# Performance work log

Measured on AMD Instinct MI355X. Metric: run time of the kernel, lower is better.

The kernel has to match this reference:

```python
import math
import jax, jax.numpy as jnp
import numpy as np

B, T, C = 4, 2048, 1024
N_HEAD = 16
HEAD_DIM = C // N_HEAD


def setup_inputs() -> dict:
    key = jax.random.key(0)
    k1, k2, k3 = jax.random.split(key, 3)
    x = jax.random.normal(k1, (B, T, C), dtype=jnp.float32)
    # nn.Linear weights: (out_features, in_features); init scale ~1/sqrt(C)
    w_attn = jax.random.normal(k2, (3 * C, C), dtype=jnp.float32) / math.sqrt(C)
    w_proj = jax.random.normal(k3, (C, C), dtype=jnp.float32) / math.sqrt(C)
    return {"x": x, "w_attn": w_attn, "w_proj": w_proj}


def reference(x, w_attn, w_proj):
    Bx, Tx, Cx = x.shape
    qkv = x @ w_attn.T  # (B,T,3C)
    q, k, v = jnp.split(qkv, 3, axis=2)
    # (B,T,H,D) -> (B,H,T,D)
    q = q.reshape(Bx, Tx, N_HEAD, HEAD_DIM).transpose(0, 2, 1, 3)
    k = k.reshape(Bx, Tx, N_HEAD, HEAD_DIM).transpose(0, 2, 1, 3)
    v = v.reshape(Bx, Tx, N_HEAD, HEAD_DIM).transpose(0, 2, 1, 3)
    scale = 1.0 / math.sqrt(HEAD_DIM)
    att = jnp.einsum("bhqd,bhkd->bhqk", q, k) * scale
    causal = jnp.tril(jnp.ones((Tx, Tx), dtype=bool))
    att = jnp.where(causal[None, None, :, :], att, -jnp.inf)
    att = jax.nn.softmax(att, axis=-1)
    out = jnp.einsum("bhqk,bhkd->bhqd", att, v)
    out = out.transpose(0, 2, 1, 3).reshape(Bx, Tx, Cx)
    return out @ w_proj.T
```

## Files before the change

kernel.cpp:

```cpp
#include <hip/hip_runtime.h>
#include <hip/hip_bf16.h>


typedef __attribute__((ext_vector_type(8))) short bf16x8;
typedef __attribute__((ext_vector_type(4))) float f32x4;
typedef __attribute__((ext_vector_type(16))) float f32x16;
typedef unsigned short ushort_t;

#if __has_builtin(__builtin_amdgcn_exp2f)
#define EXP2(x) __builtin_amdgcn_exp2f(x)
#else
#define EXP2(x) exp2f(x)
#endif

__device__ inline ushort_t f2bf(float f) {
    union { float f; unsigned int u; } x; x.f = f;
    return (ushort_t)((x.u + 0x7fffu + ((x.u >> 16) & 1u)) >> 16);
}

__device__ inline ushort_t f2bf_fast(float f) {
    union { float f; unsigned int u; } x; x.f = f;
    return (ushort_t)((x.u + 0x8000u) >> 16);
}

__device__ inline bf16x8 load8_f32_to_bf16(const float* p) {
    float4 f0 = *(const float4*)p;
    float4 f1 = *(const float4*)(p + 4);
    bf16x8 r;
    r[0] = (short)f2bf(f0.x); r[1] = (short)f2bf(f0.y);
    r[2] = (short)f2bf(f0.z); r[3] = (short)f2bf(f0.w);
    r[4] = (short)f2bf(f1.x); r[5] = (short)f2bf(f1.y);
    r[6] = (short)f2bf(f1.z); r[7] = (short)f2bf(f1.w);
    return r;
}

__device__ inline void gl2lds16(const ushort_t* g, ushort_t* l) {
    __builtin_amdgcn_global_load_lds(
        (const __attribute__((address_space(1))) unsigned int*)g,
        (__attribute__((address_space(3))) unsigned int*)l,
        16, 0, 0);
}

__global__ void cvt3(const float* __restrict__ a, long n8a,
                     const float* __restrict__ b, long n8b,
                     const float* __restrict__ c, long n8c,
                     ushort_t* __restrict__ out) {
    long i = (long)blockIdx.x * 256 + threadIdx.x;
    const float* src; long off;
    if (i < n8a) { src = a; off = i; }
    else if (i < n8a + n8b) { src = b; off = i - n8a; }
    else if (i < n8a + n8b + n8c) { src = c; off = i - n8a - n8b; }
    else return;
    *(bf16x8*)(out + i * 8) = load8_f32_to_bf16(src + off * 8);
}

__global__ void fill_zero_f32(float* out, int n) {
    int i = blockIdx.x * 256 + threadIdx.x;
    if (i < n) out[i] = 0.0f;
}

#define BM 128
#define BN 128
#define BK 64

#define QK_LOG2E_SCALE 0.18033688011112042f

template <int EPI>
__global__ __launch_bounds__(256) void gemm_lds(
        const ushort_t* __restrict__ A, const ushort_t* __restrict__ B,
        void* __restrict__ Cp, void* __restrict__ Cp2,
        int M, int N, int K) {
    __shared__ ushort_t As[BM * BK];
    __shared__ ushort_t Bs[BN * BK];

    const int tid  = threadIdx.x;
    const int lane = tid & 63;
    const int w    = tid >> 6;
    const int l31  = lane & 31;
    const int half = lane >> 5;

    const int bm = blockIdx.y * BM;
    const int bn = blockIdx.x * BN;
    const int wm = (w & 1) * 64;
    const int wn = (w >> 1) * 64;

    const int lr8 = lane >> 3;
    const int cbg = ((lane & 7) ^ lr8) * 8;
    const ushort_t* Aw = A + (size_t)(bm + w * 32 + lr8) * K + cbg;
    const ushort_t* Bw = B + (size_t)(bn + w * 32 + lr8) * K + cbg;
    ushort_t* Asw = &As[(w * 32) * BK];
    ushort_t* Bsw = &Bs[(w * 32) * BK];

    f32x16 acc[2][2] = {};

    for (int k0 = 0; k0 < K; k0 += BK) {
        if (k0) __syncthreads();
#pragma unroll
        for (int j = 0; j < 4; j++) {
            gl2lds16(Aw + (size_t)(j * 8) * K + k0, Asw + j * 8 * BK);
            gl2lds16(Bw + (size_t)(j * 8) * K + k0, Bsw + j * 8 * BK);
        }
        __syncthreads();

#pragma unroll
        for (int s = 0; s < 4; s++) {
            const int cs = (((2 * s + half) ^ (lane & 7)) * 8);
            bf16x8 af[2], bfr[2];
#pragma unroll
            for (int i = 0; i < 2; i++)
                af[i] = *(const bf16x8*)&As[(wm + i * 32 + l31) * BK + cs];
#pragma unroll
            for (int i = 0; i < 2; i++)
                bfr[i] = *(const bf16x8*)&Bs[(wn + i * 32 + l31) * BK + cs];
#pragma unroll
            for (int mi = 0; mi < 2; mi++)
#pragma unroll
                for (int ni = 0; ni < 2; ni++)
                    acc[mi][ni] = __builtin_amdgcn_mfma_f32_32x32x16_bf16(
                        af[mi], bfr[ni], acc[mi][ni], 0, 0, 0);
        }
    }

#pragma unroll
    for (int mi = 0; mi < 2; mi++)
#pragma unroll
        for (int ni = 0; ni < 2; ni++) {
            const int colg = bn + wn + ni * 32 + l31;
            if constexpr (EPI == 1) {
                float* cb = (float*)Cp + colg;
#pragma unroll
                for (int r = 0; r < 16; r++) {
                    const int row = bm + wm + mi * 32 + (r & 3) + 8 * (r >> 2) + 4 * half;
                    cb[(size_t)row * N] = acc[mi][ni][r];
                }
            } else {
                if (colg < 2048) {
                    const float qs = (colg < 1024) ? QK_LOG2E_SCALE : 1.0f;
                    ushort_t* cb = (ushort_t*)Cp + colg;
#pragma unroll
                    for (int r = 0; r < 16; r++) {
                        const int row = bm + wm + mi * 32 + (r & 3) + 8 * (r >> 2) + 4 * half;
                        cb[(size_t)row * 2048] = f2bf(acc[mi][ni][r] * qs);
                    }
                } else {
                    const int vc = colg - 2048;
                    const int hh = vc >> 6, dd = vc & 63;
                    ushort_t* vtp = (ushort_t*)Cp2 + ((size_t)hh * 64 + dd) * 2048;
#pragma unroll
                    for (int r = 0; r < 16; r++) {
                        const int row = bm + wm + mi * 32 + (r & 3) + 8 * (r >> 2) + 4 * half;
                        const int bb = row >> 11, tt = row & 2047;
                        vtp[(size_t)bb * 16 * 64 * 2048 + tt] = f2bf(acc[mi][ni][r]);
                    }
                }
            }
        }
}

#define LDK 72

template <bool A_F32, bool B_F32, int EPI>
__global__ __launch_bounds__(256) void gemm_nt(
        const void* __restrict__ Ap, const void* __restrict__ Bp,
        void* __restrict__ Cp, void* __restrict__ Cp2,
        int M, int N, int K) {
    __shared__ ushort_t As[BM * LDK];
    __shared__ ushort_t Bs[BN * LDK];

    const int tid  = threadIdx.x;
    const int lane = tid & 63;
    const int w    = tid >> 6;
    const int quad = lane >> 4;
    const int l16  = lane & 15;

    const int bm = blockIdx.y * BM;
    const int bn = blockIdx.x * BN;
    const int wm = (w & 1) * 64;
    const int wn = (w >> 1) * 64;

    f32x4 acc[4][4] = {};

    const int lrow = tid >> 3;
    const int lcol = (tid & 7) * 8;

    bf16x8 pa[4], pb[4];
#pragma unroll
    for (int i = 0; i < 4; i++) {
        const int ra = lrow + i * 32;
        if constexpr (A_F32)
            pa[i] = load8_f32_to_bf16((const float*)Ap + (size_t)(bm + ra) * K + lcol);
        else
            pa[i] = *(const bf16x8*)((const ushort_t*)Ap + (size_t)(bm + ra) * K + lcol);
        if constexpr (B_F32)
            pb[i] = load8_f32_to_bf16((const float*)Bp + (size_t)(bn + ra) * K + lcol);
        else
            pb[i] = *(const bf16x8*)((const ushort_t*)Bp + (size_t)(bn + ra) * K + lcol);
    }

    for (int k0 = 0; k0 < K; k0 += BK) {
        __syncthreads();
#pragma unroll
        for (int i = 0; i < 4; i++) {
            *(bf16x8*)&As[(lrow + i * 32) * LDK + lcol] = pa[i];
            *(bf16x8*)&Bs[(lrow + i * 32) * LDK + lcol] = pb[i];
        }
        __syncthreads();

        if (k0 + BK < K) {
            const int kn = k0 + BK + lcol;
#pragma unroll
            for (int i = 0; i < 4; i++) {
                const int ra = lrow + i * 32;
                if constexpr (A_F32)
                    pa[i] = load8_f32_to_bf16((const float*)Ap + (size_t)(bm + ra) * K + kn);
                else
                    pa[i] = *(const bf16x8*)((const ushort_t*)Ap + (size_t)(bm + ra) * K + kn);
                if constexpr (B_F32)
                    pb[i] = load8_f32_to_bf16((const float*)Bp + (size_t)(bn + ra) * K + kn);
                else
                    pb[i] = *(const bf16x8*)((const ushort_t*)Bp + (size_t)(bn + ra) * K + kn);
            }
        }

#pragma unroll
        for (int ks = 0; ks < BK; ks += 32) {
            bf16x8 af[4], bfr[4];
#pragma unroll
            for (int i = 0; i < 4; i++)
                af[i] = *(const bf16x8*)&As[(wm + i * 16 + l16) * LDK + ks + quad * 8];
#pragma unroll
            for (int i = 0; i < 4; i++)
                bfr[i] = *(const bf16x8*)&Bs[(wn + i * 16 + l16) * LDK + ks + quad * 8];
#pragma unroll
            for (int mi = 0; mi < 4; mi++)
#pragma unroll
                for (int ni = 0; ni < 4; ni++)
                    acc[mi][ni] = __builtin_amdgcn_mfma_f32_16x16x32_bf16(
                        af[mi], bfr[ni], acc[mi][ni], 0, 0, 0);
        }
    }

#pragma unroll
    for (int mi = 0; mi < 4; mi++) {
        const int row0 = bm + wm + mi * 16 + quad * 4;
#pragma unroll
        for (int r = 0; r < 4; r++) {
            const int row = row0 + r;
            if constexpr (EPI == 1) {
                float* crow = (float*)Cp + (size_t)row * N + bn + wn;
#pragma unroll
                for (int ni = 0; ni < 4; ni++)
                    crow[ni * 16 + l16] = acc[mi][ni][r];
            } else {
                if (bn < 2048) {
                    const float qs = (bn < 1024) ? QK_LOG2E_SCALE : 1.0f;
                    ushort_t* crow = (ushort_t*)Cp + (size_t)row * 2048 + bn + wn;
#pragma unroll
                    for (int ni = 0; ni < 4; ni++)
                        crow[ni * 16 + l16] = f2bf(acc[mi][ni][r] * qs);
                } else {
                    ushort_t* vt = (ushort_t*)Cp2;
                    const int bb = row >> 11, tt = row & 2047;
#pragma unroll
                    for (int ni = 0; ni < 4; ni++) {
                        const int vc = bn + wn + ni * 16 + l16 - 2048;
                        const int hh = vc >> 6, dd = vc & 63;
                        vt[(((size_t)bb * 16 + hh) * 64 + dd) * 2048 + tt] =
                            f2bf(acc[mi][ni][r]);
                    }
                }
            }
        }
    }
}

#define AT_T 2048
#define PLD 72

__global__ __launch_bounds__(256) void attn4(
        const ushort_t* __restrict__ qk,
        const ushort_t* __restrict__ vt,
        ushort_t* __restrict__ attout) {
    const int bh   = blockIdx.x;
    const int qblk = (gridDim.y - 1) - blockIdx.y;
    const int b    = bh >> 4;
    const int h    = bh & 15;

    const int tid  = threadIdx.x;
    const int lane = tid & 63;
    const int w    = tid >> 6;
    const int quad = lane >> 4;
    const int l16  = lane & 15;
    const int sw   = l16 & 7;

    __shared__ ushort_t Ks[64 * 64];
    __shared__ ushort_t Vs[80 * 64];
    __shared__ ushort_t Ps[4][32 * PLD];

    for (int i = tid; i < 16 * 64; i += 256) Vs[64 * 64 + i] = 0;
    if (tid < 64) Vs[64 * 64 + tid] = 0x3F80;

    const ushort_t* qp = qk + (size_t)b * AT_T * 2048 + h * 64;
    const ushort_t* kp = qp + 1024;
    const ushort_t* vp = vt + (size_t)bh * 64 * 2048;

    const int Q0 = qblk * 128 + w * 16;

    bf16x8 aq[2][2];
#pragma unroll
    for (int s = 0; s < 2; s++) {
        const ushort_t* qrow = qp + (size_t)(Q0 + s * 64 + l16) * 2048;
        aq[s][0] = *(const bf16x8*)(qrow + quad * 8);
        aq[s][1] = *(const bf16x8*)(qrow + 32 + quad * 8);
    }

    f32x4 o[2][5] = {};

    const int lr8 = lane >> 3;
    const int cbg = ((lane & 7) ^ lr8) * 8;

    const int nk = 2 * qblk + 2;
    for (int kt = 0; kt < nk; kt++) {
        const int k0 = kt * 64;
        if (kt) __syncthreads();
#pragma unroll
        for (int j = 0; j < 2; j++) {
            gl2lds16(kp + (size_t)(k0 + w * 16 + j * 8 + lr8) * 2048 + cbg,
                     &Ks[(w * 16 + j * 8) * 64]);
            gl2lds16(vp + (size_t)(w * 16 + j * 8 + lr8) * 2048 + k0 + cbg,
                     &Vs[(w * 16 + j * 8) * 64]);
        }
        __syncthreads();

        f32x4 s0[4], s1[4];
#pragma unroll
        for (int c = 0; c < 4; c++) {
            s0[c][0] = -8.0f; s0[c][1] = -8.0f; s0[c][2] = -8.0f; s0[c][3] = -8.0f;
            s1[c] = s0[c];
#pragma unroll
            for (int ks = 0; ks < 2; ks++) {
                const int cs = ((quad + 4 * ks) ^ sw) * 8;
                bf16x8 bk = *(const bf16x8*)&Ks[(c * 16 + l16) * 64 + cs];
                s0[c] = __builtin_amdgcn_mfma_f32_16x16x32_bf16(aq[0][ks], bk, s0[c], 0, 0, 0);
                s1[c] = __builtin_amdgcn_mfma_f32_16x16x32_bf16(aq[1][ks], bk, s1[c], 0, 0, 0);
            }
        }

        if (kt >= 2 * qblk) {
            const int q0r = Q0 + quad * 4;
#pragma unroll
            for (int c = 0; c < 4; c++) {
                const int kcol = k0 + c * 16 + l16;
#pragma unroll
                for (int r = 0; r < 4; r++)
                    if (kcol > q0r + r) s0[c][r] = -__builtin_inff();
            }
        }
        if (kt == 2 * qblk + 1) {
            const int q1r = Q0 + 64 + quad * 4;
#pragma unroll
            for (int c = 0; c < 4; c++) {
                const int kcol = k0 + c * 16 + l16;
#pragma unroll
                for (int r = 0; r < 4; r++)
                    if (kcol > q1r + r) s1[c][r] = -__builtin_inff();
            }
        }

#pragma unroll
        for (int c = 0; c < 4; c++)
#pragma unroll
            for (int r = 0; r < 4; r++) {
                Ps[w][(quad * 4 + r) * PLD + c * 16 + l16] = f2bf_fast(EXP2(s0[c][r]));
                Ps[w][(16 + quad * 4 + r) * PLD + c * 16 + l16] = f2bf_fast(EXP2(s1[c][r]));
            }

        __asm__ __volatile__("s_waitcnt lgkmcnt(0)" ::: "memory");

#pragma unroll
        for (int ks = 0; ks < 2; ks++) {
            const int cs = ((quad + 4 * ks) ^ sw) * 8;
            bf16x8 ap0 = *(const bf16x8*)&Ps[w][l16 * PLD + ks * 32 + quad * 8];
            bf16x8 ap1 = *(const bf16x8*)&Ps[w][(16 + l16) * PLD + ks * 32 + quad * 8];
#pragma unroll
            for (int n = 0; n < 5; n++) {
                bf16x8 bv = *(const bf16x8*)&Vs[(n * 16 + l16) * 64 + cs];
                o[0][n] = __builtin_amdgcn_mfma_f32_16x16x32_bf16(ap0, bv, o[0][n], 0, 0, 0);
                o[1][n] = __builtin_amdgcn_mfma_f32_16x16x32_bf16(ap1, bv, o[1][n], 0, 0, 0);
            }
        }
    }

#pragma unroll
    for (int s = 0; s < 2; s++) {
        ushort_t* op = attout + (size_t)(b * AT_T + Q0 + s * 64 + quad * 4) * 1024 + h * 64;
#pragma unroll
        for (int r = 0; r < 4; r++) {
            const float l = __shfl(o[s][4][r], lane & 48, 64);
            const float inv = 1.0f / fmaxf(l, 1e-30f);
            ushort_t* orow = op + (size_t)r * 1024;
#pragma unroll
            for (int n = 0; n < 4; n++)
                orow[n * 16 + l16] = f2bf(o[s][n][r] * inv);
        }
    }
}

extern "C" void kernel_launch(void* const* d_in, const int* in_sizes, int n_in,
                              void* d_out, int out_size, void* d_ws, size_t ws_size,
                              hipStream_t stream) {
    const float* x      = (const float*)d_in[0];
    const float* w_attn = (const float*)d_in[1];
    const float* w_proj = (const float*)d_in[2];
    float* out = (float*)d_out;

    const int M = 8192, C = 1024;
    const size_t E_QK  = (size_t)M * 2048;
    const size_t E_VT  = (size_t)4 * 16 * 64 * 2048;
    const size_t E_ATT = (size_t)M * 1024;
    const size_t E_X   = (size_t)M * 1024;
    const size_t E_WA  = (size_t)3072 * 1024;
    const size_t E_WP  = (size_t)1024 * 1024;
    const size_t need_mid  = (E_QK + E_VT + E_ATT) * 2;
    const size_t need_full = need_mid + (E_X + E_WA + E_WP) * 2;

    if (ws_size < need_mid) {
        fill_zero_f32<<<(out_size + 255) / 256, 256, 0, stream>>>(out, out_size);
        return;
    }

    ushort_t* qk  = (ushort_t*)d_ws;
    ushort_t* vt  = qk + E_QK;
    ushort_t* att = vt + E_VT;

    if (ws_size >= need_full) {
        ushort_t* xb  = att + E_ATT;
        const long n8x = (long)(E_X / 8), n8a = (long)(E_WA / 8), n8p = (long)(E_WP / 8);
        const long n8  = n8x + n8a + n8p;
        cvt3<<<(int)((n8 + 255) / 256), 256, 0, stream>>>(
            x, n8x, w_attn, n8a, w_proj, n8p, xb);

        ushort_t* wab = xb + E_X;
        ushort_t* wpb = wab + E_WA;
        gemm_lds<2><<<dim3(3 * C / BN, M / BM), 256, 0, stream>>>(
            xb, wab, qk, vt, M, 3 * C, C);
        attn4<<<dim3(64, 16), 256, 0, stream>>>(qk, vt, att);
        gemm_lds<1><<<dim3(C / BN, M / BM), 256, 0, stream>>>(
            att, wpb, out, nullptr, M, C, C);
    } else {
        gemm_nt<true, true, 2><<<dim3(3 * C / BN, M / BM), 256, 0, stream>>>(
            x, w_attn, qk, vt, M, 3 * C, C);
        attn4<<<dim3(64, 16), 256, 0, stream>>>(qk, vt, att);
        gemm_nt<false, true, 1><<<dim3(C / BN, M / BM), 256, 0, stream>>>(
            att, w_proj, out, nullptr, M, C, C);
    }
}
```

Baseline: 233.9 us.

## Add 256x256-tile 8-wave QKV GEMM with 4-stage direct-to-LDS pipeline

Replaces the 128x128 LDS GEMM for the QKV projection with a new 512-thread kernel on 256x256 tiles. It uses a 4-deep ring of direct global-to-LDS loads with K-step 32, interleaves the A and B staging with two MFMA half-phases, and raises wave priority around the MFMA blocks. An XCD-aware block-index swizzle is meant to improve L2 reuse. The goal is to hide load latency and raise MFMA utilization, at the cost of much larger LDS use (128KB) and register pressure, which may limit occupancy.

```diff
diff --git a/kernel.cpp b/kernel.cpp
--- a/kernel.cpp
+++ b/kernel.cpp
@@ -65,6 +65,135 @@
 
 #define QK_LOG2E_SCALE 0.18033688011112042f
 
+#define GBK 32
+
+__global__ __launch_bounds__(512, 2) void gemm_qkv_8p(
+        const ushort_t* __restrict__ A, const ushort_t* __restrict__ B,
+        ushort_t* __restrict__ qk, ushort_t* __restrict__ vt,
+        int M, int N, int K) {
+    __shared__ ushort_t S[4 * 2 * 256 * GBK];
+
+    const int tid  = threadIdx.x;
+    const int lane = tid & 63;
+    const int w    = tid >> 6;
+    const int quad = lane >> 4;
+    const int l16  = lane & 15;
+    const int wr   = w >> 2;
+    const int wc   = w & 3;
+
+    const int nbx = N >> 8;
+    const int cpx = gridDim.x >> 3;
+    const int swz = ((int)blockIdx.x & 7) * cpx + ((int)blockIdx.x >> 3);
+    const int bm = (swz / nbx) << 8;
+    const int bn = (swz % nbx) << 8;
+
+    const int nt = K >> 5;
+
+    const ushort_t* Ag = A + (size_t)(bm + w * 16 + (lane >> 2)) * K + (lane & 3) * 8;
+    const ushort_t* Bg = B + (size_t)(bn + w * 16 + (lane >> 2)) * K + (lane & 3) * 8;
+    const size_t rstep = (size_t)128 * K;
+
+    auto stageA = [&](int kt) {
+        ushort_t* d = S + (kt & 3) * 16384;
+        const ushort_t* g = Ag + (size_t)kt * GBK;
+        gl2lds16(g,         d + w * 512);
+        gl2lds16(g + rstep, d + 4096 + w * 512);
+    };
+    auto stageB = [&](int kt) {
+        ushort_t* d = S + (kt & 3) * 16384 + 8192;
+        const ushort_t* g = Bg + (size_t)kt * GBK;
+        gl2lds16(g,         d + w * 512);
+        gl2lds16(g + rstep, d + 4096 + w * 512);
+    };
+
+    const int aoff = (wr * 128 + l16) * GBK + quad * 8;
+    const int boff = 8192 + (wc * 64 + l16) * GBK + quad * 8;
+
+    f32x4 acc[8][4] = {};
+
+    stageA(0); stageB(0);
+    stageA(1); stageB(1);
+    stageA(2); stageB(2);
+    __asm__ __volatile__("s_waitcnt vmcnt(8)" ::: "memory");
+    __builtin_amdgcn_s_barrier();
+
+    for (int kt = 0; kt < nt; kt++) {
+        const ushort_t* Sb = S + (kt & 3) * 16384;
+        bf16x8 af[4], bfr[4];
+
+#pragma unroll
+        for (int i = 0; i < 4; i++)
+            af[i]  = *(const bf16x8*)(Sb + aoff + i * (16 * GBK));
+#pragma unroll
+        for (int i = 0; i < 4; i++)
+            bfr[i] = *(const bf16x8*)(Sb + boff + i * (16 * GBK));
+        if (kt + 3 < nt) stageA(kt + 3);
+        __builtin_amdgcn_s_barrier();
+        __builtin_amdgcn_s_setprio(1);
+#pragma unroll
+        for (int mi = 0; mi < 4; mi++)
+#pragma unroll
+            for (int ni = 0; ni < 4; ni++)
+                acc[mi][ni] = __builtin_amdgcn_mfma_f32_16x16x32_bf16(
+                    af[mi], bfr[ni], acc[mi][ni], 0, 0, 0);
+        __builtin_amdgcn_s_setprio(0);
+        __builtin_amdgcn_s_barrier();
+
+#pragma unroll
+        for (int i = 0; i < 4; i++)
+            af[i] = *(const bf16x8*)(Sb + aoff + (i + 4) * (16 * GBK));
+        if (kt + 3 < nt) stageB(kt + 3);
+        __builtin_amdgcn_s_barrier();
+        __builtin_amdgcn_s_setprio(1);
+#pragma unroll
+        for (int mi = 0; mi < 4; mi++)
+#pragma unroll
+            for (int ni = 0; ni < 4; ni++)
+                acc[mi + 4][ni] = __builtin_amdgcn_mfma_f32_16x16x32_bf16(
+                    af[mi], bfr[ni], acc[mi + 4][ni], 0, 0, 0);
+        __builtin_amdgcn_s_setprio(0);
+
+        if (kt + 3 < nt)
+            __asm__ __volatile__("s_waitcnt vmcnt(8)" ::: "memory");
+        else if (kt + 2 < nt)
+            __asm__ __volatile__("s_waitcnt vmcnt(4)" ::: "memory");
+        else if (kt + 1 < nt)
+            __asm__ __volatile__("s_waitcnt vmcnt(0)" ::: "memory");
+        __builtin_amdgcn_s_barrier();
+    }
+
+    const int colbase = bn + wc * 64;
+    const int rowbase = bm + wr * 128 + quad * 4;
+    if (colbase < 2048) {
+        const float qs = (colbase < 1024) ? QK_LOG2E_SCALE : 1.0f;
+#pragma unroll
+        for (int mi = 0; mi < 8; mi++) {
+            const int row = rowbase + mi * 16;
+            ushort_t* qp = qk + (size_t)row * 2048 + colbase + l16;
+#pragma unroll
+            for (int r = 0; r < 4; r++)
+#pragma unroll
+                for (int ni = 0; ni < 4; ni++)
+                    qp[(size_t)r * 2048 + ni * 16] = f2bf(acc[mi][ni][r] * qs);
+        }
+    } else {
+#pragma unroll
+        for (int mi = 0; mi < 8; mi++) {
+            const int row = rowbase + mi * 16;
+            const int bb = row >> 11, tt = row & 2047;
+#pragma unroll
+            for (int ni = 0; ni < 4; ni++) {
+                const int vc = colbase + ni * 16 + l16 - 2048;
+                const int hh = vc >> 6, dd = vc & 63;
+                ushort_t* vp = vt + ((((size_t)bb * 16 + hh) * 64 + dd) * 2048) + tt;
+#pragma unroll
+                for (int r = 0; r < 4; r++)
+                    vp[r] = f2bf(acc[mi][ni][r]);
+            }
+        }
+    }
+}
+
 template <int EPI>
 __global__ __launch_bounds__(256) void gemm_lds(
         const ushort_t* __restrict__ A, const ushort_t* __restrict__ B,
@@ -442,7 +571,7 @@
 
         ushort_t* wab = xb + E_X;
         ushort_t* wpb = wab + E_WA;
-        gemm_lds<2><<<dim3(3 * C / BN, M / BM), 256, 0, stream>>>(
+        gemm_qkv_8p<<<dim3((M / 256) * (3 * C / 256)), 512, 0, stream>>>(
             xb, wab, qk, vt, M, 3 * C, C);
         attn4<<<dim3(64, 16), 256, 0, stream>>>(qk, vt, att);
         gemm_lds<1><<<dim3(C / BN, M / BM), 256, 0, stream>>>(
```

Result: slower. 248.8 us (+6.4%).

## Replace bf16 GEMM with 4-stage pipelined 128x256 tile kernel with block swizzle

Applied to the files above, without the earlier changes.

Replaces the single-buffered 128x128 LDS GEMM with a 512-thread 128x256 tile kernel. It uses a 4-deep ring of direct global-to-LDS copies with BK=32 and vmcnt-based waits, so loads overlap MFMA work with one barrier per k-step. It also switches to 16x16x32 MFMAs, raises wave priority around the MFMA block, and swizzles block indices to improve L2 reuse. The aim is to hide load latency that the old load-sync-compute loop exposed. In exchange, LDS use and register pressure go up, and the unswizzled LDS layout may cause bank conflicts.

```diff
diff --git a/kernel.cpp b/kernel.cpp
--- a/kernel.cpp
+++ b/kernel.cpp
@@ -4,7 +4,6 @@
 
 typedef __attribute__((ext_vector_type(8))) short bf16x8;
 typedef __attribute__((ext_vector_type(4))) float f32x4;
-typedef __attribute__((ext_vector_type(16))) float f32x16;
 typedef unsigned short ushort_t;
 
 #if __has_builtin(__builtin_amdgcn_exp2f)
@@ -59,104 +58,134 @@
     if (i < n) out[i] = 0.0f;
 }
 
+#define QK_LOG2E_SCALE 0.18033688011112042f
+
+#define PBK 32
+#define PBUF 12288
+
+template <int EPI>
+__global__ __launch_bounds__(512) void gemm_np(
+        const ushort_t* __restrict__ A, const ushort_t* __restrict__ B,
+        void* __restrict__ Cp, void* __restrict__ Cp2,
+        int M, int N, int K) {
+    __shared__ ushort_t S[4 * PBUF];
+
+    const int tid  = threadIdx.x;
+    const int lane = tid & 63;
+    const int w    = tid >> 6;
+    const int quad = lane >> 4;
+    const int l16  = lane & 15;
+    const int wr   = w >> 2;
+    const int wc   = w & 3;
+
+    const int nbx = N >> 8;
+    const int cpx = gridDim.x >> 3;
+    const int swz = ((int)blockIdx.x & 7) * cpx + ((int)blockIdx.x >> 3);
+    const int bm = (swz / nbx) << 7;
+    const int bn = (swz % nbx) << 8;
+
+    const int nt = K >> 5;
+
+    const ushort_t* Ag = A + (size_t)(bm + w * 16 + (lane >> 2)) * K + (lane & 3) * 8;
+    const ushort_t* Bg = B + (size_t)(bn + w * 16 + (lane >> 2)) * K + (lane & 3) * 8;
+    const size_t rstep = (size_t)128 * K;
+
+    auto stage = [&](int kt) {
+        ushort_t* d = S + (kt & 3) * PBUF;
+        const size_t ko = (size_t)kt * PBK;
+        gl2lds16(Ag + ko,         d + w * 512);
+        gl2lds16(Bg + ko,         d + 4096 + w * 512);
+        gl2lds16(Bg + rstep + ko, d + 8192 + w * 512);
+    };
+
+    const int aoff = (wr * 64 + l16) * PBK + quad * 8;
+    const int boff = 4096 + (wc * 64 + l16) * PBK + quad * 8;
+
+    f32x4 acc[4][4] = {};
+
+    stage(0); stage(1); stage(2);
+    __asm__ __volatile__("s_waitcnt vmcnt(6)" ::: "memory");
+    __builtin_amdgcn_s_barrier();
+
+    for (int kt = 0; kt < nt; kt++) {
+        if (kt + 3 < nt) stage(kt + 3);
+
+        const ushort_t* Sb = S + (kt & 3) * PBUF;
+        bf16x8 af[4], bfr[4];
+#pragma unroll
+        for (int i = 0; i < 4; i++)
+            af[i]  = *(const bf16x8*)(Sb + aoff + i * (16 * PBK));
+#pragma unroll
+        for (int i = 0; i < 4; i++)
+            bfr[i] = *(const bf16x8*)(Sb + boff + i * (16 * PBK));
+
+        __builtin_amdgcn_s_setprio(1);
+#pragma unroll
+        for (int mi = 0; mi < 4; mi++)
+#pragma unroll
+            for (int ni = 0; ni < 4; ni++)
+                acc[mi][ni] = __builtin_amdgcn_mfma_f32_16x16x32_bf16(
+                    af[mi], bfr[ni], acc[mi][ni], 0, 0, 0);
+        __builtin_amdgcn_s_setprio(0);
+
+        if (kt + 3 < nt)
+            __asm__ __volatile__("s_waitcnt vmcnt(6)" ::: "memory");
+        else if (kt + 2 < nt)
+            __asm__ __volatile__("s_waitcnt vmcnt(3)" ::: "memory");
+        else if (kt + 1 < nt)
+            __asm__ __volatile__("s_waitcnt vmcnt(0)" ::: "memory");
+        __builtin_amdgcn_s_barrier();
+    }
+
+    const int colbase = bn + wc * 64;
+    const int rowbase = bm + wr * 64 + quad * 4;
+    if constexpr (EPI == 1) {
+#pragma unroll
+        for (int mi = 0; mi < 4; mi++) {
+            const int row = rowbase + mi * 16;
+            float* cr = (float*)Cp + (size_t)row * N + colbase + l16;
+#pragma unroll
+            for (int r = 0; r < 4; r++)
+#pragma unroll
+                for (int ni = 0; ni < 4; ni++)
+                    cr[(size_t)r * N + ni * 16] = acc[mi][ni][r];
+        }
+    } else {
+        if (colbase < 2048) {
+            const float qs = (colbase < 1024) ? QK_LOG2E_SCALE : 1.0f;
+#pragma unroll
+            for (int mi = 0; mi < 4; mi++) {
+                const int row = rowbase + mi * 16;
+                ushort_t* qp = (ushort_t*)Cp + (size_t)row * 2048 + colbase + l16;
+#pragma unroll
+                for (int r = 0; r < 4; r++)
+#pragma unroll
+                    for (int ni = 0; ni < 4; ni++)
+                        qp[(size_t)r * 2048 + ni * 16] = f2bf(acc[mi][ni][r] * qs);
+            }
+        } else {
+#pragma unroll
+            for (int mi = 0; mi < 4; mi++) {
+                const int row = rowbase + mi * 16;
+                const int bb = row >> 11, tt = row & 2047;
+#pragma unroll
+                for (int ni = 0; ni < 4; ni++) {
+                    const int vc = colbase + ni * 16 + l16 - 2048;
+                    const int hh = vc >> 6, dd = vc & 63;
+                    ushort_t* vp = (ushort_t*)Cp2 +
+                        ((((size_t)bb * 16 + hh) * 64 + dd) * 2048) + tt;
+#pragma unroll
+                    for (int r = 0; r < 4; r++)
+                        vp[r] = f2bf(acc[mi][ni][r]);
+                }
+            }
+        }
+    }
+}
+
 #define BM 128
 #define BN 128
 #define BK 64
-
-#define QK_LOG2E_SCALE 0.18033688011112042f
-
-template <int EPI>
-__global__ __launch_bounds__(256) void gemm_lds(
-        const ushort_t* __restrict__ A, const ushort_t* __restrict__ B,
-        void* __restrict__ Cp, void* __restrict__ Cp2,
-        int M, int N, int K) {
-    __shared__ ushort_t As[BM * BK];
-    __shared__ ushort_t Bs[BN * BK];
-
-    const int tid  = threadIdx.x;
-    const int lane = tid & 63;
-    const int w    = tid >> 6;
-    const int l31  = lane & 31;
-    const int half = lane >> 5;
-
-    const int bm = blockIdx.y * BM;
-    const int bn = blockIdx.x * BN;
-    const int wm = (w & 1) * 64;
-    const int wn = (w >> 1) * 64;
-
-    const int lr8 = lane >> 3;
-    const int cbg = ((lane & 7) ^ lr8) * 8;
-    const ushort_t* Aw = A + (size_t)(bm + w * 32 + lr8) * K + cbg;
-    const ushort_t* Bw = B + (size_t)(bn + w * 32 + lr8) * K + cbg;
-    ushort_t* Asw = &As[(w * 32) * BK];
-    ushort_t* Bsw = &Bs[(w * 32) * BK];
-
-    f32x16 acc[2][2] = {};
-
-    for (int k0 = 0; k0 < K; k0 += BK) {
-        if (k0) __syncthreads();
-#pragma unroll
-        for (int j = 0; j < 4; j++) {
-            gl2lds16(Aw + (size_t)(j * 8) * K + k0, Asw + j * 8 * BK);
-            gl2lds16(Bw + (size_t)(j * 8) * K + k0, Bsw + j * 8 * BK);
-        }
-        __syncthreads();
-
-#pragma unroll
-        for (int s = 0; s < 4; s++) {
-            const int cs = (((2 * s + half) ^ (lane & 7)) * 8);
-            bf16x8 af[2], bfr[2];
-#pragma unroll
-            for (int i = 0; i < 2; i++)
-                af[i] = *(const bf16x8*)&As[(wm + i * 32 + l31) * BK + cs];
-#pragma unroll
-            for (int i = 0; i < 2; i++)
-                bfr[i] = *(const bf16x8*)&Bs[(wn + i * 32 + l31) * BK + cs];
-#pragma unroll
-            for (int mi = 0; mi < 2; mi++)
-#pragma unroll
-                for (int ni = 0; ni < 2; ni++)
-                    acc[mi][ni] = __builtin_amdgcn_mfma_f32_32x32x16_bf16(
-                        af[mi], bfr[ni], acc[mi][ni], 0, 0, 0);
-        }
-    }
-
-#pragma unroll
-    for (int mi = 0; mi < 2; mi++)
-#pragma unroll
-        for (int ni = 0; ni < 2; ni++) {
-            const int colg = bn + wn + ni * 32 + l31;
-            if constexpr (EPI == 1) {
-                float* cb = (float*)Cp + colg;
-#pragma unroll
-                for (int r = 0; r < 16; r++) {
-                    const int row = bm + wm + mi * 32 + (r & 3) + 8 * (r >> 2) + 4 * half;
-                    cb[(size_t)row * N] = acc[mi][ni][r];
-                }
-            } else {
-                if (colg < 2048) {
-                    const float qs = (colg < 1024) ? QK_LOG2E_SCALE : 1.0f;
-                    ushort_t* cb = (ushort_t*)Cp + colg;
-#pragma unroll
-                    for (int r = 0; r < 16; r++) {
-                        const int row = bm + wm + mi * 32 + (r & 3) + 8 * (r >> 2) + 4 * half;
-                        cb[(size_t)row * 2048] = f2bf(acc[mi][ni][r] * qs);
-                    }
-                } else {
-                    const int vc = colg - 2048;
-                    const int hh = vc >> 6, dd = vc & 63;
-                    ushort_t* vtp = (ushort_t*)Cp2 + ((size_t)hh * 64 + dd) * 2048;
-#pragma unroll
-                    for (int r = 0; r < 16; r++) {
-                        const int row = bm + wm + mi * 32 + (r & 3) + 8 * (r >> 2) + 4 * half;
-                        const int bb = row >> 11, tt = row & 2047;
-                        vtp[(size_t)bb * 16 * 64 * 2048 + tt] = f2bf(acc[mi][ni][r]);
-                    }
-                }
-            }
-        }
-}
-
 #define LDK 72
 
 template <bool A_F32, bool B_F32, int EPI>
@@ -442,10 +471,10 @@
 
         ushort_t* wab = xb + E_X;
         ushort_t* wpb = wab + E_WA;
-        gemm_lds<2><<<dim3(3 * C / BN, M / BM), 256, 0, stream>>>(
+        gemm_np<2><<<dim3((M / 128) * (3 * C / 256)), 512, 0, stream>>>(
             xb, wab, qk, vt, M, 3 * C, C);
         attn4<<<dim3(64, 16), 256, 0, stream>>>(qk, vt, att);
-        gemm_lds<1><<<dim3(C / BN, M / BM), 256, 0, stream>>>(
+        gemm_np<1><<<dim3((M / 128) * (C / 256)), 512, 0, stream>>>(
             att, wpb, out, nullptr, M, C, C);
     } else {
         gemm_nt<true, true, 2><<<dim3(3 * C / BN, M / BM), 256, 0, stream>>>(
```

After: 238.7 us. 1.02x slower.
